# Optimization experiments

Measured on AMD Instinct MI355X. Metric: run time of the kernel, lower is better.

Reference implementation:

```python
import jax, jax.numpy as jnp
import numpy as np

DIM = 256
HEADS = 8
HEAD_DIM = DIM // HEADS
WS = 7            # window size
SHIFT = 3         # shift size
H = 56
W = 56
B = 32
WA = WS * WS      # window area = 49
NWH, NWW = H // WS, W // WS
NW = NWH * NWW    # windows per image


def _make_attn_mask():
    # replicate the torch mask construction for the shifted windows
    img = np.zeros((H, W), dtype=np.float32)
    cnt = 0
    for hs in (slice(0, -WS), slice(-WS, -SHIFT), slice(-SHIFT, None)):
        for ws_ in (slice(0, -WS), slice(-WS, -SHIFT), slice(-SHIFT, None)):
            img[hs, ws_] = cnt
            cnt += 1
    mw = img.reshape(NWH, WS, NWW, WS).transpose(0, 2, 1, 3).reshape(-1, WA)  # (nW, 49)
    diff = mw[:, None, :] - mw[:, :, None]                                    # (nW, 49, 49)
    return np.where(diff != 0, -100.0, 0.0).astype(np.float32)


def _make_rel_index():
    coords = np.stack(np.meshgrid(np.arange(WS), np.arange(WS), indexing='ij')).reshape(2, -1)
    rel = coords[:, :, None] - coords[:, None, :]        # (2, 49, 49)
    rel = rel.transpose(1, 2, 0) + (WS - 1)              # shift to >= 0
    rel[..., 0] *= 2 * WS - 1
    return rel.sum(-1).astype(np.int32)                  # (49, 49) in [0, 169)


def setup_inputs() -> dict:
    key = jax.random.key(0)
    ks = jax.random.split(key, 12)
    s = 0.02
    inp = {
        'x': jax.random.normal(ks[0], (B, H, W, DIM), dtype=jnp.float32),
        'ln1_w': jnp.ones((DIM,), jnp.float32), 'ln1_b': jnp.zeros((DIM,), jnp.float32),
        'qkv_w': s * jax.random.normal(ks[1], (3 * DIM, DIM), jnp.float32),
        'qkv_b': jnp.zeros((3 * DIM,), jnp.float32),
        'rpb_table': s * jax.random.normal(ks[2], ((2 * WS - 1) ** 2, HEADS), jnp.float32),
        'proj_w': s * jax.random.normal(ks[3], (DIM, DIM), jnp.float32),
        'proj_b': jnp.zeros((DIM,), jnp.float32),
        'ln2_w': jnp.ones((DIM,), jnp.float32), 'ln2_b': jnp.zeros((DIM,), jnp.float32),
        'fc1_w': s * jax.random.normal(ks[4], (4 * DIM, DIM), jnp.float32),
        'fc1_b': jnp.zeros((4 * DIM,), jnp.float32),
        'ln3_w': jnp.ones((4 * DIM,), jnp.float32), 'ln3_b': jnp.zeros((4 * DIM,), jnp.float32),
        'fc2_w': s * jax.random.normal(ks[5], (DIM, 4 * DIM), jnp.float32),
        'fc2_b': jnp.zeros((DIM,), jnp.float32),
        'attn_mask': jnp.asarray(_make_attn_mask()),     # (nW, 49, 49)
        'rel_index': jnp.asarray(_make_rel_index()),     # (49, 49) int32
    }
    return inp


def _ln(x, w, b, eps=1e-5):
    m = jnp.mean(x, axis=-1, keepdims=True)
    v = jnp.mean((x - m) ** 2, axis=-1, keepdims=True)
    return (x - m) * jax.lax.rsqrt(v + eps) * w + b


def reference(x, ln1_w, ln1_b, qkv_w, qkv_b, rpb_table, proj_w, proj_b,
              ln2_w, ln2_b, fc1_w, fc1_b, ln3_w, ln3_b, fc2_w, fc2_b,
              attn_mask, rel_index):
    Bn, Hn, Wn, C = x.shape
    # ---- attention branch ----
    y = _ln(x, ln1_w, ln1_b)
    sh = jnp.roll(y, (-SHIFT, -SHIFT), axis=(1, 2))
    # window partition: (B, H, W, C) -> (B*nW, 49, C)
    win = sh.reshape(Bn, NWH, WS, NWW, WS, C).transpose(0, 1, 3, 2, 4, 5).reshape(Bn * NW, WA, C)
    qkv = win @ qkv_w.T + qkv_b                              # (Bw, 49, 3C)
    qkv = qkv.reshape(Bn * NW, WA, 3, HEADS, HEAD_DIM).transpose(2, 0, 3, 1, 4)
    q, k, v = qkv[0], qkv[1], qkv[2]                         # (Bw, h, 49, d)
    scale = HEAD_DIM ** -0.5
    attn = jnp.einsum('bhqd,bhkd->bhqk', q * scale, k)       # (Bw, h, 49, 49)
    bias = rpb_table[rel_index]                              # (49, 49, h)
    attn = attn + jnp.transpose(bias, (2, 0, 1))[None]
    attn = attn.reshape(Bn, NW, HEADS, WA, WA) + attn_mask[None, :, None]
    attn = jax.nn.softmax(attn, axis=-1).reshape(Bn * NW, HEADS, WA, WA)
    out = jnp.einsum('bhqk,bhkd->bhqd', attn, v)             # (Bw, h, 49, d)
    out = out.transpose(0, 2, 1, 3).reshape(Bn * NW, WA, C)
    out = out @ proj_w.T + proj_b
    # window reverse + un-shift
    out = out.reshape(Bn, NWH, NWW, WS, WS, C).transpose(0, 1, 3, 2, 4, 5).reshape(Bn, Hn, Wn, C)
    out = jnp.roll(out, (SHIFT, SHIFT), axis=(1, 2))
    x = x + out
    # ---- MLP branch (note: extra LayerNorm inside MLP per source) ----
    z = _ln(x, ln2_w, ln2_b)
    h = jax.nn.gelu(z @ fc1_w.T + fc1_b, approximate=False)
    h = _ln(h, ln3_w, ln3_b)
    x = x + (h @ fc2_w.T + fc2_b)
    return x
```

## Files before the change

kernel.cpp:

```cpp
#include <hip/hip_runtime.h>
#include <hip/hip_bf16.h>
#include <math.h>

typedef __attribute__((ext_vector_type(8))) short bf16x8;
typedef __attribute__((ext_vector_type(4))) float f32x4;
typedef __attribute__((ext_vector_type(4))) float f4;
typedef __attribute__((ext_vector_type(8))) unsigned short us8;
typedef __attribute__((ext_vector_type(4))) unsigned short us4;
typedef unsigned short u16;
typedef unsigned int u32;

#define HEADS 8
#define SHIFT_ 3
#define HIMG 56
#define WIMG 56
#define WA 49
#define NTOK 100352
#define NPAIR 16384

static __device__ __forceinline__ float bf2f(u16 v){ return __uint_as_float(((u32)v)<<16); }
static __device__ __forceinline__ u16 f2bf(float f){
  u32 u = __float_as_uint(f);
  return (u16)((u + 0x7fffu + ((u>>16)&1u)) >> 16);
}
static __device__ __forceinline__ u32 pkbf(float a, float b){
  __hip_bfloat162 h = __float22bfloat162_rn(make_float2(a, b));
  return *reinterpret_cast<u32*>(&h);
}
static __device__ __forceinline__ float wsum(float v){
  #pragma unroll
  for (int off=32; off>0; off>>=1) v += __shfl_xor(v, off, 64);
  return v;
}
static __device__ __forceinline__ void glds16(const u16* g, u16* l){
  __builtin_amdgcn_global_load_lds(
      (const __attribute__((address_space(1))) unsigned int*)g,
      (__attribute__((address_space(3))) unsigned int*)l, 16, 0, 0);
}
static __device__ __forceinline__ int tok2pix(int row){
  int bw = row / 49, t = row - bw*49;
  int b  = bw >> 6,  w = bw & 63;
  int wh = w >> 3,   ww = w & 7;
  int th = t / 7,    tw = t - th*7;
  int r = wh*7 + th + SHIFT_; if (r >= HIMG) r -= HIMG;
  int c = ww*7 + tw + SHIFT_; if (c >= WIMG) c -= WIMG;
  return (b*HIMG + r)*WIMG + c;
}
static __device__ __forceinline__ float gelu_f(float x){
  float e = __expf(-1.702f*x);
  return x*__builtin_amdgcn_rcpf(1.0f+e);
}

template<int C, int ISBF>
__global__ void ln_stats_kernel(const void* __restrict__ srcv, float* __restrict__ stats){
  int wave = threadIdx.x >> 6, lane = threadIdx.x & 63;
  int tok = blockIdx.x*4 + wave;
  float s=0.f, s2=0.f;
  if (ISBF == 0){
    const float* p = (const float*)srcv + (size_t)tok*C;
    #pragma unroll
    for (int i=0;i<C/256;i++){
      f4 v = *(const f4*)(p + lane*4*(C/256) + i*4);
      #pragma unroll
      for (int e=0;e<4;e++){ float f=v[e]; s+=f; s2+=f*f; }
    }
  } else {
    const u16* p = (const u16*)srcv + (size_t)tok*C;
    #pragma unroll
    for (int i=0;i<C/512;i++){
      us8 v = *(const us8*)(p + lane*8*(C/512) + i*8);
      #pragma unroll
      for (int e=0;e<8;e++){ float f=bf2f(v[e]); s+=f; s2+=f*f; }
    }
  }
  s = wsum(s); s2 = wsum(s2);
  if (lane==0){
    float mean = s/(float)C;
    float var  = s2/(float)C - mean*mean;
    stats[2*tok]   = mean;
    stats[2*tok+1] = rsqrtf(var + 1e-5f);
  }
}

__global__ void ln_apply_kernel(const float* __restrict__ src, u16* __restrict__ dst){
  int wave = threadIdx.x >> 6, lane = threadIdx.x & 63;
  int tok = blockIdx.x*4 + wave;
  const float* p = src + (size_t)tok*256;
  f4 a = *(const f4*)(p + lane*4);
  float s = a[0]+a[1]+a[2]+a[3];
  float s2 = a[0]*a[0]+a[1]*a[1]+a[2]*a[2]+a[3]*a[3];
  s = wsum(s); s2 = wsum(s2);
  float mean = s*(1.f/256.f);
  float var  = s2*(1.f/256.f) - mean*mean;
  float rstd = rsqrtf(var + 1e-5f);
  u32 o2[2];
  o2[0] = pkbf((a[0]-mean)*rstd, (a[1]-mean)*rstd);
  o2[1] = pkbf((a[2]-mean)*rstd, (a[3]-mean)*rstd);
  *(u32*)(dst + (size_t)tok*256 + lane*4)     = o2[0];
  *(u32*)(dst + (size_t)tok*256 + lane*4 + 2) = o2[1];
}

__global__ void ln_apply_b_kernel(const u16* __restrict__ src, u16* __restrict__ dst,
                                  float* __restrict__ st){
  int wave = threadIdx.x >> 6, lane = threadIdx.x & 63;
  int tok = blockIdx.x*4 + wave;
  const u16* p = src + (size_t)tok*256 + lane*4;
  us4 a4 = *(const us4*)p;
  float a0=bf2f(a4[0]), a1=bf2f(a4[1]), a2=bf2f(a4[2]), a3=bf2f(a4[3]);
  float s = a0+a1+a2+a3;
  float s2 = a0*a0+a1*a1+a2*a2+a3*a3;
  s = wsum(s); s2 = wsum(s2);
  float mean = s*(1.f/256.f);
  float var  = s2*(1.f/256.f) - mean*mean;
  float rstd = rsqrtf(var + 1e-5f);
  u32 o0 = pkbf((a0-mean)*rstd, (a1-mean)*rstd);
  u32 o1 = pkbf((a2-mean)*rstd, (a3-mean)*rstd);
  u16* d = dst + (size_t)tok*256 + lane*4;
  *(u32*)d     = o0;
  *(u32*)(d+2) = o1;
  if (lane==0){ st[2*tok] = mean; st[2*tok+1] = rstd; }
}

__global__ void cmb_kernel(const float* __restrict__ rpb, const int* __restrict__ rel,
                           const float* __restrict__ mask, u16* __restrict__ cmb){
  int lin = blockIdx.x*1024 + threadIdx.x*4;
  int j0 = lin & 63;
  int r3 = lin >> 6;
  int i  = r3 % 49;
  int wh = r3 / 49;
  int h = wh & 7, w = wh >> 3;
  us4 o;
  #pragma unroll
  for (int e=0;e<4;e++){
    int j = j0 + e;
    float v = 0.f;
    if (j < WA) v = rpb[rel[i*WA+j]*8 + h] + mask[((size_t)w*WA + i)*WA + j];
    o[e] = f2bf(v);
  }
  *(us4*)(cmb + lin) = o;
}

__global__ void prep_weights(
    const float* __restrict__ qkv_w, const float* __restrict__ qkv_b,
    const float* __restrict__ ln1w,  const float* __restrict__ ln1b,
    const float* __restrict__ fc1_w, const float* __restrict__ fc1_b,
    const float* __restrict__ ln2w,  const float* __restrict__ ln2b,
    const float* __restrict__ fc2_w, const float* __restrict__ fc2_b,
    const float* __restrict__ ln3w,  const float* __restrict__ ln3b,
    const float* __restrict__ proj_w, const float* __restrict__ proj_b,
    u16* __restrict__ wq, float* __restrict__ bq,
    u16* __restrict__ w1, float* __restrict__ b1,
    u16* __restrict__ w2, float* __restrict__ b2,
    u16* __restrict__ wp, float* __restrict__ bp,
    float* __restrict__ cs2, float* __restrict__ hstats)
{
  for (int idx = blockIdx.x*256 + threadIdx.x; idx < 2*NTOK; idx += gridDim.x*256)
    hstats[idx] = 0.f;

  int wave = threadIdx.x>>6, lane = threadIdx.x&63;
  int n = blockIdx.x*4 + wave;
  const float *W,*lw,*lb,*bs; u16* WO; float* BO; int K, row, noln, docs;
  float qs = 1.f;
  if (n < 768)      { W=qkv_w; lw=ln1w; lb=ln1b; bs=qkv_b; WO=wq; BO=bq; K=256;  row=n;      noln=0; docs=0;
                      if (n < 256) qs = 0.17677669529663689f; }
  else if (n < 1792){ W=fc1_w; lw=ln2w; lb=ln2b; bs=fc1_b; WO=w1; BO=b1; K=256;  row=n-768;  noln=0; docs=0; }
  else if (n < 2048){ W=fc2_w; lw=ln3w; lb=ln3b; bs=fc2_b; WO=w2; BO=b2; K=1024; row=n-1792; noln=0; docs=1; }
  else              { W=proj_w; lw=nullptr; lb=nullptr; bs=proj_b; WO=wp; BO=bp; K=256; row=n-2048; noln=1; docs=0; }
  float dot = 0.f, cs = 0.f;
  for (int k=lane; k<K; k+=64){
    float wv = W[(size_t)row*K + k];
    if (noln){
      WO[(size_t)row*K + k] = f2bf(wv);
    } else {
      dot += wv * lb[k];
      u16 q = f2bf(wv * lw[k] * qs);
      WO[(size_t)row*K + k] = q;
      cs += bf2f(q);
    }
  }
  dot = wsum(dot);
  if (docs){ cs = wsum(cs); if (lane==0) cs2[row] = cs; }
  if (lane==0) BO[row] = (bs[row] + dot) * qs;
}

template<int SMODE, int EPI, int SWAP, int DEPTH>
__global__ __launch_bounds__(256)
void gemm18(const void* __restrict__ Av, const u16* __restrict__ Bt,
            const float* __restrict__ stats, float* __restrict__ hstats,
            const float* __restrict__ biasf, const float* __restrict__ resid,
            const float* __restrict__ colsum, void* __restrict__ outv,
            int K, int NT, int CHUNK)
{
  constexpr int BM=128, BN=128, BK=32;
  constexpr int NBUF = DEPTH + 1;
  __shared__ u16 smem[NBUF*8192];
  constexpr int BOFF = NBUF*4096;
  int b = blockIdx.x;
  int linear = (b & 7)*CHUNK + (b >> 3);
  int mt = linear / NT, nt = linear - mt*NT;
  int m0 = mt*BM, n0 = nt*BN;
  int tid  = threadIdx.x;
  int lane = tid & 63, wave = tid >> 6;
  int wr = wave >> 1, wc = wave & 1;
  int lc16 = lane & 15, g = lane >> 4;
  int nsteps = K >> 5;

  const u16* asrc[2];
  const u16* bsrc[2];
  #pragma unroll
  for (int i=0;i<2;i++){
    int c = tid + i*256;
    int row = c >> 2, gch = ((c & 3) - (row >> 1)) & 3;
    if (SMODE <= 1){
      int grow = (SMODE==0) ? tok2pix(m0+row) : (m0+row);
      asrc[i] = (const u16*)Av + (size_t)grow*K + gch*8;
    }
    bsrc[i] = Bt + (size_t)(n0+row)*K + gch*8;
  }
  float smean[2], srstd[2];
  if (SMODE == 3){
    #pragma unroll
    for (int i=0;i<2;i++){
      int grow = m0 + ((tid + i*256) >> 2);
      smean[i] = stats[2*grow]; srstd[i] = stats[2*grow+1];
    }
  }

  f32x4 acc[4][4];
  #pragma unroll
  for (int i=0;i<4;i++)
    #pragma unroll
    for (int j=0;j<4;j++){ acc[i][j][0]=0.f; acc[i][j][1]=0.f; acc[i][j][2]=0.f; acc[i][j][3]=0.f; }

  if (SMODE <= 1){
    #pragma unroll
    for (int pt=0; pt<DEPTH; ++pt){
      int kt = pt << 5;
      #pragma unroll
      for (int i=0;i<2;i++) glds16(asrc[i]+kt, smem + pt*4096 + i*2048 + wave*512);
      #pragma unroll
      for (int i=0;i<2;i++) glds16(bsrc[i]+kt, smem + BOFF + pt*4096 + i*2048 + wave*512);
    }
    if (DEPTH == 3)      asm volatile("s_waitcnt vmcnt(8)" ::: "memory");
    else                 asm volatile("s_waitcnt vmcnt(4)" ::: "memory");
    __builtin_amdgcn_s_barrier();

    int cur = 0;
    for (int t=0; t<nsteps; ++t){
      if (t+DEPTH < nsteps){
        int ktD = (t+DEPTH) << 5;
        int nb = cur + DEPTH; if (nb >= NBUF) nb -= NBUF;
        int off = nb*4096;
        #pragma unroll
        for (int i=0;i<2;i++) glds16(asrc[i]+ktD, smem + off + i*2048 + wave*512);
        #pragma unroll
        for (int i=0;i<2;i++) glds16(bsrc[i]+ktD, smem + BOFF + off + i*2048 + wave*512);
      }
      const u16* Ap = smem + cur*4096;
      const u16* Bp = smem + BOFF + cur*4096;
      bf16x8 af[4], bfr[4];
      #pragma unroll
      for (int mi=0;mi<4;mi++){
        int r = wr*64 + mi*16 + lc16;
        u32 byte = (u32)(r*64) + ((u32)((g + (r>>1)) & 3) << 4);
        af[mi] = *(const bf16x8*)(Ap + (byte>>1));
      }
      #pragma unroll
      for (int ni=0;ni<4;ni++){
        int r = wc*64 + ni*16 + lc16;
        u32 byte = (u32)(r*64) + ((u32)((g + (r>>1)) & 3) << 4);
        bfr[ni] = *(const bf16x8*)(Bp + (byte>>1));
      }
      #pragma unroll
      for (int mi=0;mi<4;mi++)
        #pragma unroll
        for (int ni=0;ni<4;ni++)
          acc[mi][ni] = SWAP ? __builtin_amdgcn_mfma_f32_16x16x32_bf16(bfr[ni], af[mi], acc[mi][ni], 0, 0, 0)
                             : __builtin_amdgcn_mfma_f32_16x16x32_bf16(af[mi], bfr[ni], acc[mi][ni], 0, 0, 0);
      int rem = nsteps - 1 - t;
      int cnt = (rem < DEPTH) ? rem : DEPTH;
      if (cnt >= 3)      asm volatile("s_waitcnt vmcnt(8)" ::: "memory");
      else if (cnt == 2) asm volatile("s_waitcnt vmcnt(4)" ::: "memory");
      else if (cnt == 1) asm volatile("s_waitcnt vmcnt(0)" ::: "memory");
      __builtin_amdgcn_s_barrier();
      cur = (cur+1 == NBUF) ? 0 : cur+1;
    }
  } else {
    f4 rcurf[2][2];
    #pragma unroll
    for (int i=0;i<2;i++){
      int c = tid + i*256; int row = c>>2, gch = ((c&3) - (row>>1)) & 3;
      const float* ap = (const float*)Av + (size_t)(m0+row)*K + gch*8;
      rcurf[i][0] = *(const f4*)ap; rcurf[i][1] = *(const f4*)(ap+4);
    }
    for (int t=0; t<nsteps; ++t){
      int kt = t << 5;
      #pragma unroll
      for (int i=0;i<2;i++){
        int c = tid + i*256; int row = c>>2, s = c&3;
        us8 o;
        #pragma unroll
        for (int e=0;e<8;e++){
          float fv = rcurf[i][e>>2][e&3];
          o[e] = f2bf((fv - smean[i])*srstd[i]);
        }
        u32 byte = (u32)(row*64) + ((u32)s << 4);
        *(us8*)(smem + (byte>>1)) = o;
      }
      #pragma unroll
      for (int i=0;i<2;i++) glds16(bsrc[i]+kt, smem + BOFF + i*2048 + wave*512);
      __syncthreads();
      if (t+1 < nsteps){
        int kt1 = kt + 32;
        #pragma unroll
        for (int i=0;i<2;i++){
          int c = tid + i*256; int row = c>>2, gch = ((c&3) - (row>>1)) & 3;
          const float* ap = (const float*)Av + (size_t)(m0+row)*K + kt1 + gch*8;
          rcurf[i][0] = *(const f4*)ap; rcurf[i][1] = *(const f4*)(ap+4);
        }
      }
      bf16x8 af[4], bfr[4];
      #pragma unroll
      for (int mi=0;mi<4;mi++){
        int r = wr*64 + mi*16 + lc16;
        u32 byte = (u32)(r*64) + ((u32)((g + (r>>1)) & 3) << 4);
        af[mi] = *(const bf16x8*)(smem + (byte>>1));
      }
      #pragma unroll
      for (int ni=0;ni<4;ni++){
        int r = wc*64 + ni*16 + lc16;
        u32 byte = (u32)(r*64) + ((u32)((g + (r>>1)) & 3) << 4);
        bfr[ni] = *(const bf16x8*)(smem + BOFF + (byte>>1));
      }
      #pragma unroll
      for (int mi=0;mi<4;mi++)
        #pragma unroll
        for (int ni=0;ni<4;ni++)
          acc[mi][ni] = SWAP ? __builtin_amdgcn_mfma_f32_16x16x32_bf16(bfr[ni], af[mi], acc[mi][ni], 0, 0, 0)
                             : __builtin_amdgcn_mfma_f32_16x16x32_bf16(af[mi], bfr[ni], acc[mi][ni], 0, 0, 0);
      __syncthreads();
    }
  }

  int lr = lane >> 4;
  if (EPI==0){
    u16* Cs = smem;
    #pragma unroll
    for (int mi=0;mi<4;mi++){
      #pragma unroll
      for (int ni=0;ni<4;ni++){
        int cl = wc*64 + ni*16 + lc16;
        float bv = biasf[n0 + cl];
        #pragma unroll
        for (int j=0;j<4;j++){
          int rl = wr*64 + mi*16 + lr*4 + j;
          float v = acc[mi][ni][j] + bv;
          u32 byte = (u32)(rl*256 + cl*2) ^ ((u32)(rl&7)<<4);
          Cs[byte>>1] = f2bf(v);
        }
      }
    }
    __syncthreads();
    #pragma unroll
    for (int i=0;i<8;i++){
      int c = tid + i*256;
      int rl = c>>4, c0 = (c&15)*8;
      u32 byte = (u32)(rl*256 + c0*2) ^ ((u32)(rl&7)<<4);
      us8 v = *(const us8*)(Cs + (byte>>1));
      int row = m0 + rl, col = n0 + c0;
      int which = col>>8, hh = (col>>5)&7, d0 = col&31;
      int bwi = row/49, t = row - bwi*49;
      *(us8*)((u16*)outv + ((size_t)which*NPAIR + bwi*8 + hh)*(WA*32) + t*32 + d0) = v;
    }
  } else if (EPI==2){
    u16* Cs = smem;
    #pragma unroll
    for (int mi=0;mi<4;mi++){
      int rl = wr*64 + mi*16 + lc16;
      float ss = 0.f, sq = 0.f;
      #pragma unroll
      for (int ni=0;ni<4;ni++){
        int cl = wc*64 + ni*16 + g*4;
        f4 bv = *(const f4*)(biasf + n0 + cl);
        float v0 = gelu_f(acc[mi][ni][0] + bv[0]);
        float v1 = gelu_f(acc[mi][ni][1] + bv[1]);
        float v2 = gelu_f(acc[mi][ni][2] + bv[2]);
        float v3 = gelu_f(acc[mi][ni][3] + bv[3]);
        ss += (v0+v1)+(v2+v3);
        sq += (v0*v0+v1*v1)+(v2*v2+v3*v3);
        u32 w0 = pkbf(v0, v1), w1 = pkbf(v2, v3);
        u32 byte = (u32)(rl*256 + cl*2) ^ ((u32)(rl&7)<<4);
        *(u32*)(Cs + (byte>>1))     = w0;
        *(u32*)(Cs + (byte>>1) + 2) = w1;
      }
      ss += __shfl_xor(ss, 16, 64); ss += __shfl_xor(ss, 32, 64);
      sq += __shfl_xor(sq, 16, 64); sq += __shfl_xor(sq, 32, 64);
      if (g==0){
        int grow = m0 + rl;
        atomicAdd(&hstats[2*grow],   ss);
        atomicAdd(&hstats[2*grow+1], sq);
      }
    }
    __syncthreads();
    #pragma unroll
    for (int i=0;i<8;i++){
      int c = tid + i*256;
      int rl = c>>4, c0 = (c&15)*8;
      u32 byte = (u32)(rl*256 + c0*2) ^ ((u32)(rl&7)<<4);
      us8 v = *(const us8*)(Cs + (byte>>1));
      int row = m0 + rl, col = n0 + c0;
      *(us8*)((u16*)outv + (size_t)row*1024 + col) = v;
    }
  } else if (EPI==5){
    u16* Cs = smem;
    #pragma unroll
    for (int mi=0;mi<4;mi++){
      int rl = wr*64 + mi*16 + lc16;
      int pix = tok2pix(m0 + rl);
      #pragma unroll
      for (int ni=0;ni<4;ni++){
        int cl = wc*64 + ni*16 + g*4;
        int col = n0 + cl;
        f4 bv = *(const f4*)(biasf + col);
        f4 rr = *(const f4*)(resid + (size_t)pix*256 + col);
        float v0 = acc[mi][ni][0] + bv[0] + rr[0];
        float v1 = acc[mi][ni][1] + bv[1] + rr[1];
        float v2 = acc[mi][ni][2] + bv[2] + rr[2];
        float v3 = acc[mi][ni][3] + bv[3] + rr[3];
        u32 w0 = pkbf(v0, v1), w1 = pkbf(v2, v3);
        u32 byte = (u32)(rl*256 + cl*2) ^ ((u32)(rl&7)<<4);
        *(u32*)(Cs + (byte>>1))     = w0;
        *(u32*)(Cs + (byte>>1) + 2) = w1;
      }
    }
    __syncthreads();
    #pragma unroll
    for (int i=0;i<8;i++){
      int c = tid + i*256;
      int rl = c>>4, c0 = (c&15)*8;
      u32 byte = (u32)(rl*256 + c0*2) ^ ((u32)(rl&7)<<4);
      us8 v = *(const us8*)(Cs + (byte>>1));
      int pix = tok2pix(m0 + rl);
      *(us8*)((u16*)outv + (size_t)pix*256 + n0 + c0) = v;
    }
  } else {
    #pragma unroll
    for (int mi=0;mi<4;mi++){
      int rl = wr*64 + mi*16 + lc16;
      int grow = m0 + rl;
      float rs = 1.f, mr = 0.f, istd2 = 0.f, mean2 = 0.f;
      if (EPI==4 || EPI==6){
        float s = stats[2*grow], q = stats[2*grow+1];
        float mean = s*(1.f/1024.f);
        float var  = q*(1.f/1024.f) - mean*mean;
        rs = rsqrtf(var + 1e-5f);
        mr = mean*rs;
      }
      if (EPI==6){
        mean2 = hstats[2*grow];
        istd2 = __builtin_amdgcn_rcpf(hstats[2*grow+1]);
      }
      size_t rowbase = (EPI==1) ? (size_t)tok2pix(grow)*256 : (size_t)grow*256;
      #pragma unroll
      for (int ni=0;ni<4;ni++){
        int col = n0 + wc*64 + ni*16 + g*4;
        f4 bv = *(const f4*)(biasf + col);
        f4 v;
        if (EPI==4 || EPI==6){
          f4 cw = *(const f4*)(colsum + col);
          #pragma unroll
          for (int j=0;j<4;j++) v[j] = acc[mi][ni][j]*rs - mr*cw[j] + bv[j];
        } else {
          #pragma unroll
          for (int j=0;j<4;j++) v[j] = acc[mi][ni][j] + bv[j];
        }
        if (EPI==6){
          us4 xr = *(const us4*)((const u16*)resid + rowbase + col);
          #pragma unroll
          for (int j=0;j<4;j++) v[j] += bf2f(xr[j])*istd2 + mean2;
        } else {
          f4 rr = *(const f4*)(resid + rowbase + col);
          v += rr;
        }
        *(f4*)((float*)outv + rowbase + col) = v;
      }
    }
  }
}

__global__ __launch_bounds__(128)
void attn_mfma_kernel(
    const u16* __restrict__ qkv,
    const u16* __restrict__ cmb,
    u16* __restrict__ outb)
{
  __shared__ u16 smem2[2][12288];
  int wave = threadIdx.x>>6, lane = threadIdx.x&63;
  int pairbase = blockIdx.x*4 + wave*2;
  int bw = pairbase>>3, h0 = pairbase&7, w = bw&63;
  int lc = lane&15, g = lane>>4;
  u16* S = &smem2[wave][0];
  const u16* qg0 = qkv + (size_t)pairbase*(WA*32);
  const u16* qg1 = qg0 + WA*32;
  const u16* kg0 = qg0 + (size_t)NPAIR*(WA*32);
  const u16* kg1 = kg0 + WA*32;
  const u16* vg0 = qg0 + (size_t)2*NPAIR*(WA*32);
  const u16* vg1 = vg0 + WA*32;

  #pragma unroll
  for (int i=0;i<4;i++){
    int idx = i*64 + lane;
    if (idx < 196){
      glds16(kg0 + idx*8, S + idx*8);
      glds16(kg1 + idx*8, S + 2048 + idx*8);
    }
  }
  us8 vv0[4], vv1[4];
  #pragma unroll
  for (int i=0;i<4;i++){
    int idx = i*64+lane; int r = idx>>2, seg = idx&3;
    if (r < WA){
      vv0[i] = *(const us8*)(vg0 + r*32 + seg*8);
      vv1[i] = *(const us8*)(vg1 + r*32 + seg*8);
    } else {
      #pragma unroll
      for (int e=0;e<8;e++){ vv0[i][e]=0; vv1[i][e]=0; }
    }
  }
  bf16x8 qa0[4], qa1[4];
  #pragma unroll
  for (int mi=0;mi<4;mi++){
    int r = mi*16 + lc;
    if (r < WA){
      qa0[mi] = *(const bf16x8*)(qg0 + r*32 + g*8);
      qa1[mi] = *(const bf16x8*)(qg1 + r*32 + g*8);
    } else {
      bf16x8 z;
      #pragma unroll
      for (int e=0;e<8;e++) z[e]=0;
      qa0[mi]=z; qa1[mi]=z;
    }
  }
  #pragma unroll
  for (int i=0;i<4;i++){
    int idx = i*64+lane; int r = idx>>2, seg = idx&3;
    #pragma unroll
    for (int e=0;e<8;e++){
      int d = seg*8 + e;
      u32 byte = ((u32)(d*128 + r*2)) ^ ((u32)(d&7)<<4);
      S[4096 + (byte>>1)] = vv0[i][e];
      S[6144 + (byte>>1)] = vv1[i][e];
    }
  }
  asm volatile("s_waitcnt vmcnt(0)" ::: "memory");
  __builtin_amdgcn_sched_barrier(0);

  u16* Pp = S + 8192;
  #pragma unroll
  for (int p=0; p<2; ++p){
    const u16* Kp = S + p*2048;
    const u16* Vp = S + 4096 + p*2048;
    const u16* cmbp = cmb + ((size_t)((w*8 + h0 + p)*49))*64;

    f32x4 acc[4][4];
    #pragma unroll
    for (int i=0;i<4;i++)
      #pragma unroll
      for (int j=0;j<4;j++){ acc[i][j][0]=0.f; acc[i][j][1]=0.f; acc[i][j][2]=0.f; acc[i][j][3]=0.f; }

    __builtin_amdgcn_s_setprio(1);
    #pragma unroll
    for (int ni=0;ni<4;ni++){
      bf16x8 kb = *(const bf16x8*)(Kp + (ni*16+lc)*32 + g*8);
      #pragma unroll
      for (int mi=0;mi<4;mi++)
        acc[mi][ni] = __builtin_amdgcn_mfma_f32_16x16x32_bf16(p==0 ? qa0[mi] : qa1[mi], kb, acc[mi][ni], 0, 0, 0);
    }
    __builtin_amdgcn_s_setprio(0);

    float rinv[4][4];
    #pragma unroll
    for (int mi=0;mi<4;mi++){
      #pragma unroll
      for (int jr=0;jr<4;jr++){
        int i = mi*16 + g*4 + jr;
        float sv[4];
        #pragma unroll
        for (int ni=0;ni<4;ni++){
          int j = ni*16 + lc;
          float s;
          if (i < WA && j < WA){
            s = acc[mi][ni][jr] + bf2f(cmbp[i*64 + j]);
          } else s = -1e9f;
          sv[ni] = s;
        }
        float mx = fmaxf(fmaxf(sv[0],sv[1]), fmaxf(sv[2],sv[3]));
        #pragma unroll
        for (int off=1; off<16; off<<=1) mx = fmaxf(mx, __shfl_xor(mx, off, 64));
        float sum = 0.f;
        #pragma unroll
        for (int ni=0;ni<4;ni++){ sv[ni] = __expf(sv[ni]-mx); sum += sv[ni]; }
        #pragma unroll
        for (int off=1; off<16; off<<=1) sum += __shfl_xor(sum, off, 64);
        rinv[mi][jr] = __builtin_amdgcn_rcpf(sum);
        #pragma unroll
        for (int ni=0;ni<4;ni++){
          int j = ni*16 + lc;
          u32 byte = ((u32)(i*128 + j*2)) ^ ((u32)(i&7)<<4);
          Pp[byte>>1] = f2bf(sv[ni]);
        }
      }
    }

    bf16x8 vb[2][2];
    #pragma unroll
    for (int kk=0;kk<2;kk++)
      #pragma unroll
      for (int ni=0;ni<2;ni++){
        int d = ni*16 + lc;
        u32 byte = ((u32)(d*128 + kk*64 + g*16)) ^ ((u32)(d&7)<<4);
        vb[kk][ni] = *(const bf16x8*)(Vp + (byte>>1));
      }
    f32x4 aco[4][2];
    #pragma unroll
    for (int i=0;i<4;i++)
      #pragma unroll
      for (int j=0;j<2;j++){ aco[i][j][0]=0.f; aco[i][j][1]=0.f; aco[i][j][2]=0.f; aco[i][j][3]=0.f; }
    __builtin_amdgcn_s_setprio(1);
    #pragma unroll
    for (int mi=0;mi<4;mi++){
      int r = mi*16 + lc;
      #pragma unroll
      for (int kk=0;kk<2;kk++){
        u32 byte = ((u32)(r*128 + kk*64 + g*16)) ^ ((u32)(r&7)<<4);
        bf16x8 pa = *(const bf16x8*)(Pp + (byte>>1));
        #pragma unroll
        for (int ni=0;ni<2;ni++)
          aco[mi][ni] = __builtin_amdgcn_mfma_f32_16x16x32_bf16(pa, vb[kk][ni], aco[mi][ni], 0, 0, 0);
      }
    }
    __builtin_amdgcn_s_setprio(0);

    u16* Op = S + p*2048;
    #pragma unroll
    for (int mi=0;mi<4;mi++){
      #pragma unroll
      for (int jr=0;jr<4;jr++){
        int i = mi*16 + g*4 + jr;
        if (i < WA){
          float rv = rinv[mi][jr];
          #pragma unroll
          for (int ni=0;ni<2;ni++)
            Op[i*32 + ni*16 + lc] = f2bf(aco[mi][ni][jr]*rv);
        }
      }
    }
    size_t obase = (size_t)(bw*WA)*256 + (h0+p)*32;
    #pragma unroll
    for (int i=0;i<4;i++){
      int c = i*64 + lane;
      if (c < WA*4){
        int t = c>>2, seg = c&3;
        *(us8*)(outb + obase + (size_t)t*256 + seg*8) = *(const us8*)(Op + t*32 + seg*8);
      }
    }
  }
}

extern "C" void kernel_launch(void* const* d_in, const int* in_sizes, int n_in,
                              void* d_out, int out_size, void* d_ws, size_t ws_size,
                              hipStream_t stream) {
  const float* x      = (const float*)d_in[0];
  const float* ln1w   = (const float*)d_in[1];
  const float* ln1b   = (const float*)d_in[2];
  const float* qkv_w  = (const float*)d_in[3];
  const float* qkv_b  = (const float*)d_in[4];
  const float* rpb    = (const float*)d_in[5];
  const float* proj_w = (const float*)d_in[6];
  const float* proj_b = (const float*)d_in[7];
  const float* ln2w   = (const float*)d_in[8];
  const float* ln2b   = (const float*)d_in[9];
  const float* fc1_w  = (const float*)d_in[10];
  const float* fc1_b  = (const float*)d_in[11];
  const float* ln3w   = (const float*)d_in[12];
  const float* ln3b   = (const float*)d_in[13];
  const float* fc2_w  = (const float*)d_in[14];
  const float* fc2_b  = (const float*)d_in[15];
  const float* amask  = (const float*)d_in[16];
  const int*   rel    = (const int*)d_in[17];
  float* out = (float*)d_out;

  char* ws = (char*)d_ws;
  float* hstats = (float*)(ws);
  float* stats2 = (float*)(ws +  802816);
  float* bq     = (float*)(ws + 1605632);
  float* b1     = (float*)(ws + 1608704);
  float* b2     = (float*)(ws + 1612800);
  float* bp     = (float*)(ws + 1613824);
  float* cs2    = (float*)(ws + 1614848);
  u16*   wq     = (u16*)  (ws + 1615872);
  u16*   w1     = (u16*)  (ws + 2009088);
  u16*   w2     = (u16*)  (ws + 2533376);
  u16*   wp     = (u16*)  (ws + 3057664);
  const size_t P0 = 3188736;
  u16*   qkvbuf = (u16*)(ws + P0);
  u16*   attno  = (u16*)(ws + P0 + 154140672);
  u16*   xb     = (u16*)(ws + P0 + 154140672);
  u16*   ob     = (u16*)(ws + P0);
  u16*   hbuf   = (u16*)(ws + P0);
  u16*   x1b    = (u16*)(ws + P0 + 205520896);
  u16*   cmb    = (u16*)(ws + P0 + 205520896);
  const int bigws = (ws_size >= (size_t)(P0 + 205520896ull + 51380224ull));

  prep_weights<<<576,256,0,stream>>>(qkv_w,qkv_b,ln1w,ln1b, fc1_w,fc1_b,ln2w,ln2b,
                                     fc2_w,fc2_b,ln3w,ln3b, proj_w,proj_b,
                                     wq,bq, w1,b1, w2,b2, wp,bp, cs2, hstats);
  cmb_kernel<<<1568,256,0,stream>>>(rpb, rel, amask, cmb);
  ln_apply_kernel<<<NTOK/4,256,0,stream>>>(x, xb);
  gemm18<0,0,0,2><<<784*6,256,0,stream>>>(xb, wq, nullptr, nullptr, bq, nullptr, nullptr, qkvbuf, 256, 6, 588);
  attn_mfma_kernel<<<NPAIR/4,128,0,stream>>>(qkvbuf, cmb, attno);
  if (bigws){
    gemm18<1,5,1,2><<<784*2,256,0,stream>>>(attno, wp, nullptr, nullptr, bp, x, nullptr, ob, 256, 2, 196);
    ln_apply_b_kernel<<<NTOK/4,256,0,stream>>>(ob, x1b, stats2);
    gemm18<1,2,1,2><<<784*8,256,0,stream>>>(x1b, w1, nullptr, hstats, b1, nullptr, nullptr, hbuf, 256, 8, 784);
    gemm18<1,6,1,2><<<784*2,256,0,stream>>>(hbuf, w2, hstats, stats2, b2, (const float*)x1b, cs2, out, 1024, 2, 196);
  } else {
    gemm18<1,1,1,2><<<784*2,256,0,stream>>>(attno, wp, nullptr, nullptr, bp, x, nullptr, out, 256, 2, 196);
    ln_stats_kernel<256,0><<<NTOK/4,256,0,stream>>>(out, stats2);
    gemm18<3,2,1,2><<<784*8,256,0,stream>>>(out, w1, stats2, hstats, b1, nullptr, nullptr, (u16*)(ws+P0), 256, 8, 784);
    gemm18<1,4,1,2><<<784*2,256,0,stream>>>((u16*)(ws+P0), w2, hstats, nullptr, b2, out, cs2, out, 1024, 2, 196);
  }
}
```

Baseline: 531.2 us.

## Add 256x128 tile GEMM with 512 threads for MLP fc1/fc2

Introduces gemm19, a GEMM with a 256x128 output tile, 8 waves and a 3-buffer, depth-2 global-to-LDS pipeline, and uses it for the fc1 (GELU + stats) and fc2 (LN-folded residual) GEMMs on the big-workspace path. The larger M tile doubles reuse of the B (weight) tile per block and halves the block count, with the aim of cutting LDS and global traffic per output. The existing gemm18 wait counts are simplified to assume DEPTH 2. The cost is more LDS per block and more threads per block, which may lower occupancy, and the shallower prefetch depth may expose more load latency.

```diff
diff --git a/kernel.cpp b/kernel.cpp
--- a/kernel.cpp
+++ b/kernel.cpp
@@ -241,8 +241,7 @@
       #pragma unroll
       for (int i=0;i<2;i++) glds16(bsrc[i]+kt, smem + BOFF + pt*4096 + i*2048 + wave*512);
     }
-    if (DEPTH == 3)      asm volatile("s_waitcnt vmcnt(8)" ::: "memory");
-    else                 asm volatile("s_waitcnt vmcnt(4)" ::: "memory");
+    asm volatile("s_waitcnt vmcnt(4)" ::: "memory");
     __builtin_amdgcn_s_barrier();
 
     int cur = 0;
@@ -279,8 +278,7 @@
                              : __builtin_amdgcn_mfma_f32_16x16x32_bf16(af[mi], bfr[ni], acc[mi][ni], 0, 0, 0);
       int rem = nsteps - 1 - t;
       int cnt = (rem < DEPTH) ? rem : DEPTH;
-      if (cnt >= 3)      asm volatile("s_waitcnt vmcnt(8)" ::: "memory");
-      else if (cnt == 2) asm volatile("s_waitcnt vmcnt(4)" ::: "memory");
+      if (cnt >= 2)      asm volatile("s_waitcnt vmcnt(4)" ::: "memory");
       else if (cnt == 1) asm volatile("s_waitcnt vmcnt(0)" ::: "memory");
       __builtin_amdgcn_s_barrier();
       cur = (cur+1 == NBUF) ? 0 : cur+1;
@@ -371,6 +369,38 @@
       int which = col>>8, hh = (col>>5)&7, d0 = col&31;
       int bwi = row/49, t = row - bwi*49;
       *(us8*)((u16*)outv + ((size_t)which*NPAIR + bwi*8 + hh)*(WA*32) + t*32 + d0) = v;
+    }
+  } else if (EPI==5){
+    u16* Cs = smem;
+    #pragma unroll
+    for (int mi=0;mi<4;mi++){
+      int rl = wr*64 + mi*16 + lc16;
+      int pix = tok2pix(m0 + rl);
+      #pragma unroll
+      for (int ni=0;ni<4;ni++){
+        int cl = wc*64 + ni*16 + g*4;
+        int col = n0 + cl;
+        f4 bv = *(const f4*)(biasf + col);
+        f4 rr = *(const f4*)(resid + (size_t)pix*256 + col);
+        float v0 = acc[mi][ni][0] + bv[0] + rr[0];
+        float v1 = acc[mi][ni][1] + bv[1] + rr[1];
+        float v2 = acc[mi][ni][2] + bv[2] + rr[2];
+        float v3 = acc[mi][ni][3] + bv[3] + rr[3];
+        u32 w0 = pkbf(v0, v1), w1 = pkbf(v2, v3);
+        u32 byte = (u32)(rl*256 + cl*2) ^ ((u32)(rl&7)<<4);
+        *(u32*)(Cs + (byte>>1))     = w0;
+        *(u32*)(Cs + (byte>>1) + 2) = w1;
+      }
+    }
+    __syncthreads();
+    #pragma unroll
+    for (int i=0;i<8;i++){
+      int c = tid + i*256;
+      int rl = c>>4, c0 = (c&15)*8;
+      u32 byte = (u32)(rl*256 + c0*2) ^ ((u32)(rl&7)<<4);
+      us8 v = *(const us8*)(Cs + (byte>>1));
+      int pix = tok2pix(m0 + rl);
+      *(us8*)((u16*)outv + (size_t)pix*256 + n0 + c0) = v;
     }
   } else if (EPI==2){
     u16* Cs = smem;
@@ -410,38 +440,6 @@
       us8 v = *(const us8*)(Cs + (byte>>1));
       int row = m0 + rl, col = n0 + c0;
       *(us8*)((u16*)outv + (size_t)row*1024 + col) = v;
-    }
-  } else if (EPI==5){
-    u16* Cs = smem;
-    #pragma unroll
-    for (int mi=0;mi<4;mi++){
-      int rl = wr*64 + mi*16 + lc16;
-      int pix = tok2pix(m0 + rl);
-      #pragma unroll
-      for (int ni=0;ni<4;ni++){
-        int cl = wc*64 + ni*16 + g*4;
-        int col = n0 + cl;
-        f4 bv = *(const f4*)(biasf + col);
-        f4 rr = *(const f4*)(resid + (size_t)pix*256 + col);
-        float v0 = acc[mi][ni][0] + bv[0] + rr[0];
-        float v1 = acc[mi][ni][1] + bv[1] + rr[1];
-        float v2 = acc[mi][ni][2] + bv[2] + rr[2];
-        float v3 = acc[mi][ni][3] + bv[3] + rr[3];
-        u32 w0 = pkbf(v0, v1), w1 = pkbf(v2, v3);
-        u32 byte = (u32)(rl*256 + cl*2) ^ ((u32)(rl&7)<<4);
-        *(u32*)(Cs + (byte>>1))     = w0;
-        *(u32*)(Cs + (byte>>1) + 2) = w1;
-      }
-    }
-    __syncthreads();
-    #pragma unroll
-    for (int i=0;i<8;i++){
-      int c = tid + i*256;
-      int rl = c>>4, c0 = (c&15)*8;
-      u32 byte = (u32)(rl*256 + c0*2) ^ ((u32)(rl&7)<<4);
-      us8 v = *(const us8*)(Cs + (byte>>1));
-      int pix = tok2pix(m0 + rl);
-      *(us8*)((u16*)outv + (size_t)pix*256 + n0 + c0) = v;
     }
   } else {
     #pragma unroll
@@ -482,6 +480,161 @@
           f4 rr = *(const f4*)(resid + rowbase + col);
           v += rr;
         }
+        *(f4*)((float*)outv + rowbase + col) = v;
+      }
+    }
+  }
+}
+
+template<int EPI>
+__global__ __launch_bounds__(512)
+void gemm19(const u16* __restrict__ Av, const u16* __restrict__ Bt,
+            const float* __restrict__ stats, float* __restrict__ st2,
+            const float* __restrict__ biasf, const u16* __restrict__ residb,
+            const float* __restrict__ colsum, void* __restrict__ outv,
+            int K, int NT, int CHUNK)
+{
+  constexpr int BM=256, BN=128, BK=32;
+  __shared__ u16 smem[36864];
+  int b = blockIdx.x;
+  int linear = (b & 7)*CHUNK + (b >> 3);
+  int mt = linear / NT, nt = linear - mt*NT;
+  int m0 = mt*BM, n0 = nt*BN;
+  int tid  = threadIdx.x;
+  int lane = tid & 63, wave = tid >> 6;
+  int wr = wave >> 1, wc = wave & 1;
+  int lc16 = lane & 15, g = lane >> 4;
+  int nsteps = K >> 5;
+
+  const u16* asrc[2];
+  #pragma unroll
+  for (int i=0;i<2;i++){
+    int c = tid + i*512;
+    int row = c >> 2, gch = ((c & 3) - (row >> 1)) & 3;
+    asrc[i] = Av + (size_t)(m0+row)*K + gch*8;
+  }
+  const u16* bsrc0;
+  {
+    int row = tid >> 2, gch = ((tid & 3) - (row >> 1)) & 3;
+    bsrc0 = Bt + (size_t)(n0+row)*K + gch*8;
+  }
+
+  f32x4 acc[4][4];
+  #pragma unroll
+  for (int i=0;i<4;i++)
+    #pragma unroll
+    for (int j=0;j<4;j++){ acc[i][j][0]=0.f; acc[i][j][1]=0.f; acc[i][j][2]=0.f; acc[i][j][3]=0.f; }
+
+  #pragma unroll
+  for (int pt=0; pt<2; ++pt){
+    int kt = pt << 5;
+    #pragma unroll
+    for (int i=0;i<2;i++) glds16(asrc[i]+kt, smem + pt*8192 + i*4096 + wave*512);
+    glds16(bsrc0+kt, smem + 24576 + pt*4096 + wave*512);
+  }
+  asm volatile("s_waitcnt vmcnt(3)" ::: "memory");
+  __builtin_amdgcn_s_barrier();
+
+  int cur = 0;
+  for (int t=0; t<nsteps; ++t){
+    if (t+2 < nsteps){
+      int kt2 = (t+2) << 5;
+      int nb = cur + 2; if (nb >= 3) nb -= 3;
+      #pragma unroll
+      for (int i=0;i<2;i++) glds16(asrc[i]+kt2, smem + nb*8192 + i*4096 + wave*512);
+      glds16(bsrc0+kt2, smem + 24576 + nb*4096 + wave*512);
+    }
+    const u16* Ap = smem + cur*8192;
+    const u16* Bp = smem + 24576 + cur*4096;
+    bf16x8 af[4], bfr[4];
+    #pragma unroll
+    for (int mi=0;mi<4;mi++){
+      int r = wr*64 + mi*16 + lc16;
+      u32 byte = (u32)(r*64) + ((u32)((g + (r>>1)) & 3) << 4);
+      af[mi] = *(const bf16x8*)(Ap + (byte>>1));
+    }
+    #pragma unroll
+    for (int ni=0;ni<4;ni++){
+      int r = wc*64 + ni*16 + lc16;
+      u32 byte = (u32)(r*64) + ((u32)((g + (r>>1)) & 3) << 4);
+      bfr[ni] = *(const bf16x8*)(Bp + (byte>>1));
+    }
+    #pragma unroll
+    for (int mi=0;mi<4;mi++)
+      #pragma unroll
+      for (int ni=0;ni<4;ni++)
+        acc[mi][ni] = __builtin_amdgcn_mfma_f32_16x16x32_bf16(bfr[ni], af[mi], acc[mi][ni], 0, 0, 0);
+    int rem = nsteps - 1 - t;
+    int cnt = (rem < 2) ? rem : 2;
+    if (cnt == 2)      asm volatile("s_waitcnt vmcnt(3)" ::: "memory");
+    else if (cnt == 1) asm volatile("s_waitcnt vmcnt(0)" ::: "memory");
+    __builtin_amdgcn_s_barrier();
+    cur = (cur+1 == 3) ? 0 : cur+1;
+  }
+
+  if (EPI==2){
+    u16* Cs = smem;
+    #pragma unroll
+    for (int mi=0;mi<4;mi++){
+      int rl = wr*64 + mi*16 + lc16;
+      float ss = 0.f, sq = 0.f;
+      #pragma unroll
+      for (int ni=0;ni<4;ni++){
+        int cl = wc*64 + ni*16 + g*4;
+        f4 bv = *(const f4*)(biasf + n0 + cl);
+        float v0 = gelu_f(acc[mi][ni][0] + bv[0]);
+        float v1 = gelu_f(acc[mi][ni][1] + bv[1]);
+        float v2 = gelu_f(acc[mi][ni][2] + bv[2]);
+        float v3 = gelu_f(acc[mi][ni][3] + bv[3]);
+        ss += (v0+v1)+(v2+v3);
+        sq += (v0*v0+v1*v1)+(v2*v2+v3*v3);
+        u32 w0 = pkbf(v0, v1), w1 = pkbf(v2, v3);
+        u32 byte = (u32)(rl*256 + cl*2) ^ ((u32)(rl&7)<<4);
+        *(u32*)(Cs + (byte>>1))     = w0;
+        *(u32*)(Cs + (byte>>1) + 2) = w1;
+      }
+      ss += __shfl_xor(ss, 16, 64); ss += __shfl_xor(ss, 32, 64);
+      sq += __shfl_xor(sq, 16, 64); sq += __shfl_xor(sq, 32, 64);
+      if (g==0){
+        int grow = m0 + rl;
+        atomicAdd(&st2[2*grow],   ss);
+        atomicAdd(&st2[2*grow+1], sq);
+      }
+    }
+    __syncthreads();
+    #pragma unroll
+    for (int i=0;i<8;i++){
+      int c = tid + i*512;
+      int rl = c>>4, c0 = (c&15)*8;
+      u32 byte = (u32)(rl*256 + c0*2) ^ ((u32)(rl&7)<<4);
+      us8 v = *(const us8*)(Cs + (byte>>1));
+      int row = m0 + rl, col = n0 + c0;
+      *(us8*)((u16*)outv + (size_t)row*1024 + col) = v;
+    }
+  } else {
+    #pragma unroll
+    for (int mi=0;mi<4;mi++){
+      int rl = wr*64 + mi*16 + lc16;
+      int grow = m0 + rl;
+      float s = stats[2*grow], q = stats[2*grow+1];
+      float mean = s*(1.f/1024.f);
+      float var  = q*(1.f/1024.f) - mean*mean;
+      float rs = rsqrtf(var + 1e-5f);
+      float mr = mean*rs;
+      float mean2 = st2[2*grow];
+      float istd2 = __builtin_amdgcn_rcpf(st2[2*grow+1]);
+      size_t rowbase = (size_t)grow*256;
+      #pragma unroll
+      for (int ni=0;ni<4;ni++){
+        int col = n0 + wc*64 + ni*16 + g*4;
+        f4 bv = *(const f4*)(biasf + col);
+        f4 cw = *(const f4*)(colsum + col);
+        f4 v;
+        #pragma unroll
+        for (int j=0;j<4;j++) v[j] = acc[mi][ni][j]*rs - mr*cw[j] + bv[j];
+        us4 xr = *(const us4*)(residb + rowbase + col);
+        #pragma unroll
+        for (int j=0;j<4;j++) v[j] += bf2f(xr[j])*istd2 + mean2;
         *(f4*)((float*)outv + rowbase + col) = v;
       }
     }
@@ -722,8 +875,8 @@
   if (bigws){
     gemm18<1,5,1,2><<<784*2,256,0,stream>>>(attno, wp, nullptr, nullptr, bp, x, nullptr, ob, 256, 2, 196);
     ln_apply_b_kernel<<<NTOK/4,256,0,stream>>>(ob, x1b, stats2);
-    gemm18<1,2,1,2><<<784*8,256,0,stream>>>(x1b, w1, nullptr, hstats, b1, nullptr, nullptr, hbuf, 256, 8, 784);
-    gemm18<1,6,1,2><<<784*2,256,0,stream>>>(hbuf, w2, hstats, stats2, b2, (const float*)x1b, cs2, out, 1024, 2, 196);
+    gemm19<2><<<3136,512,0,stream>>>(x1b, w1, nullptr, hstats, b1, nullptr, nullptr, hbuf, 256, 8, 392);
+    gemm19<6><<<784,512,0,stream>>>(hbuf, w2, hstats, stats2, b2, x1b, cs2, out, 1024, 2, 98);
   } else {
     gemm18<1,1,1,2><<<784*2,256,0,stream>>>(attno, wp, nullptr, nullptr, bp, x, nullptr, out, 256, 2, 196);
     ln_stats_kernel<256,0><<<NTOK/4,256,0,stream>>>(out, stats2);
```

Measured after the change: 534.6 us. About the same (+0.6%).

## Fuse fc1, GELU, LayerNorm and fc2 into a single MLP kernel

Applied to the files above, without the earlier changes.

Adds mlp_fused, which keeps a 128-row tile of the normalized activations in shared memory. It computes the 1024-wide hidden layer in 128-column chunks with GELU, accumulates the LayerNorm statistics in registers, and feeds each chunk straight into the fc2 accumulation. This removes the round trip of the large hidden buffer through global memory and the atomic statistics pass. In exchange the kernel uses 128 KB of LDS and 512 threads per block, which lowers occupancy, and it only double-buffers weights. The GEMM pipeline wait counts are also simplified so they no longer wait for fewer outstanding loads at depth 3.

```diff
diff --git a/kernel.cpp b/kernel.cpp
--- a/kernel.cpp
+++ b/kernel.cpp
@@ -241,8 +241,7 @@
       #pragma unroll
       for (int i=0;i<2;i++) glds16(bsrc[i]+kt, smem + BOFF + pt*4096 + i*2048 + wave*512);
     }
-    if (DEPTH == 3)      asm volatile("s_waitcnt vmcnt(8)" ::: "memory");
-    else                 asm volatile("s_waitcnt vmcnt(4)" ::: "memory");
+    asm volatile("s_waitcnt vmcnt(4)" ::: "memory");
     __builtin_amdgcn_s_barrier();
 
     int cur = 0;
@@ -279,8 +278,7 @@
                              : __builtin_amdgcn_mfma_f32_16x16x32_bf16(af[mi], bfr[ni], acc[mi][ni], 0, 0, 0);
       int rem = nsteps - 1 - t;
       int cnt = (rem < DEPTH) ? rem : DEPTH;
-      if (cnt >= 3)      asm volatile("s_waitcnt vmcnt(8)" ::: "memory");
-      else if (cnt == 2) asm volatile("s_waitcnt vmcnt(4)" ::: "memory");
+      if (cnt >= 2)      asm volatile("s_waitcnt vmcnt(4)" ::: "memory");
       else if (cnt == 1) asm volatile("s_waitcnt vmcnt(0)" ::: "memory");
       __builtin_amdgcn_s_barrier();
       cur = (cur+1 == NBUF) ? 0 : cur+1;
@@ -371,6 +369,38 @@
       int which = col>>8, hh = (col>>5)&7, d0 = col&31;
       int bwi = row/49, t = row - bwi*49;
       *(us8*)((u16*)outv + ((size_t)which*NPAIR + bwi*8 + hh)*(WA*32) + t*32 + d0) = v;
+    }
+  } else if (EPI==5){
+    u16* Cs = smem;
+    #pragma unroll
+    for (int mi=0;mi<4;mi++){
+      int rl = wr*64 + mi*16 + lc16;
+      int pix = tok2pix(m0 + rl);
+      #pragma unroll
+      for (int ni=0;ni<4;ni++){
+        int cl = wc*64 + ni*16 + g*4;
+        int col = n0 + cl;
+        f4 bv = *(const f4*)(biasf + col);
+        f4 rr = *(const f4*)(resid + (size_t)pix*256 + col);
+        float v0 = acc[mi][ni][0] + bv[0] + rr[0];
+        float v1 = acc[mi][ni][1] + bv[1] + rr[1];
+        float v2 = acc[mi][ni][2] + bv[2] + rr[2];
+        float v3 = acc[mi][ni][3] + bv[3] + rr[3];
+        u32 w0 = pkbf(v0, v1), w1 = pkbf(v2, v3);
+        u32 byte = (u32)(rl*256 + cl*2) ^ ((u32)(rl&7)<<4);
+        *(u32*)(Cs + (byte>>1))     = w0;
+        *(u32*)(Cs + (byte>>1) + 2) = w1;
+      }
+    }
+    __syncthreads();
+    #pragma unroll
+    for (int i=0;i<8;i++){
+      int c = tid + i*256;
+      int rl = c>>4, c0 = (c&15)*8;
+      u32 byte = (u32)(rl*256 + c0*2) ^ ((u32)(rl&7)<<4);
+      us8 v = *(const us8*)(Cs + (byte>>1));
+      int pix = tok2pix(m0 + rl);
+      *(us8*)((u16*)outv + (size_t)pix*256 + n0 + c0) = v;
     }
   } else if (EPI==2){
     u16* Cs = smem;
@@ -411,38 +441,6 @@
       int row = m0 + rl, col = n0 + c0;
       *(us8*)((u16*)outv + (size_t)row*1024 + col) = v;
     }
-  } else if (EPI==5){
-    u16* Cs = smem;
-    #pragma unroll
-    for (int mi=0;mi<4;mi++){
-      int rl = wr*64 + mi*16 + lc16;
-      int pix = tok2pix(m0 + rl);
-      #pragma unroll
-      for (int ni=0;ni<4;ni++){
-        int cl = wc*64 + ni*16 + g*4;
-        int col = n0 + cl;
-        f4 bv = *(const f4*)(biasf + col);
-        f4 rr = *(const f4*)(resid + (size_t)pix*256 + col);
-        float v0 = acc[mi][ni][0] + bv[0] + rr[0];
-        float v1 = acc[mi][ni][1] + bv[1] + rr[1];
-        float v2 = acc[mi][ni][2] + bv[2] + rr[2];
-        float v3 = acc[mi][ni][3] + bv[3] + rr[3];
-        u32 w0 = pkbf(v0, v1), w1 = pkbf(v2, v3);
-        u32 byte = (u32)(rl*256 + cl*2) ^ ((u32)(rl&7)<<4);
-        *(u32*)(Cs + (byte>>1))     = w0;
-        *(u32*)(Cs + (byte>>1) + 2) = w1;
-      }
-    }
-    __syncthreads();
-    #pragma unroll
-    for (int i=0;i<8;i++){
-      int c = tid + i*256;
-      int rl = c>>4, c0 = (c&15)*8;
-      u32 byte = (u32)(rl*256 + c0*2) ^ ((u32)(rl&7)<<4);
-      us8 v = *(const us8*)(Cs + (byte>>1));
-      int pix = tok2pix(m0 + rl);
-      *(us8*)((u16*)outv + (size_t)pix*256 + n0 + c0) = v;
-    }
   } else {
     #pragma unroll
     for (int mi=0;mi<4;mi++){
@@ -484,6 +482,209 @@
         }
         *(f4*)((float*)outv + rowbase + col) = v;
       }
+    }
+  }
+}
+
+__global__ __launch_bounds__(512)
+void mlp_fused(const u16* __restrict__ x1b, const u16* __restrict__ w1,
+               const u16* __restrict__ w2, const float* __restrict__ b1,
+               const float* __restrict__ b2, const float* __restrict__ colsum,
+               const float* __restrict__ st2, float* __restrict__ outv)
+{
+  __shared__ u16 smem[65536];
+  u16* Al = smem;
+  u16* Hl = smem + 32768;
+  u16* Db = smem + 49152;
+
+  int b = blockIdx.x;
+  int linear = (b & 7)*98 + (b >> 3);
+  int m0 = linear * 128;
+  int tid = threadIdx.x;
+  int lane = tid & 63, wave = tid >> 6;
+  int wr = wave >> 2, wcol = wave & 3;
+  int lc16 = lane & 15, g = lane >> 4;
+
+  #pragma unroll
+  for (int i=0;i<8;i++){
+    int c = tid + i*512;
+    int row = c >> 5, s = c & 31, gs = (s - row) & 31;
+    glds16(x1b + (size_t)(m0+row)*256 + gs*8, Al + i*4096 + wave*512);
+  }
+  #pragma unroll
+  for (int i=0;i<2;i++){
+    int c = tid + i*512;
+    int hrow = c >> 3, s = c & 7, gs = (s - hrow) & 7;
+    glds16(w1 + (size_t)hrow*256 + gs*8, Db + i*4096 + wave*512);
+  }
+  asm volatile("s_waitcnt vmcnt(0)" ::: "memory");
+  __builtin_amdgcn_s_barrier();
+
+  f32x4 acc2[4][4];
+  #pragma unroll
+  for (int i=0;i<4;i++)
+    #pragma unroll
+    for (int j=0;j<4;j++){ acc2[i][j][0]=0.f; acc2[i][j][1]=0.f; acc2[i][j][2]=0.f; acc2[i][j][3]=0.f; }
+  float ss[4] = {0.f,0.f,0.f,0.f};
+  float sq[4] = {0.f,0.f,0.f,0.f};
+
+  #pragma unroll 1
+  for (int n=0; n<8; ++n){
+    f32x4 acc1[4][2];
+    #pragma unroll
+    for (int i=0;i<4;i++)
+      #pragma unroll
+      for (int j=0;j<2;j++){ acc1[i][j][0]=0.f; acc1[i][j][1]=0.f; acc1[i][j][2]=0.f; acc1[i][j][3]=0.f; }
+
+    #pragma unroll
+    for (int t=0; t<4; ++t){
+      if (t < 3){
+        #pragma unroll
+        for (int i=0;i<2;i++){
+          int c = tid + i*512;
+          int hrow = c >> 3, s = c & 7, gs = (s - hrow) & 7;
+          glds16(w1 + (size_t)(n*128+hrow)*256 + (t+1)*64 + gs*8,
+                 Db + ((t+1)&1)*8192 + i*4096 + wave*512);
+        }
+      } else {
+        #pragma unroll
+        for (int i=0;i<2;i++){
+          int c = tid + i*512;
+          int crow = c >> 2, s = c & 3, gs = (s - crow) & 3;
+          glds16(w2 + (size_t)crow*1024 + n*128 + gs*8,
+                 Db + i*4096 + wave*512);
+        }
+      }
+      const u16* Bp = Db + (t&1)*8192;
+      #pragma unroll
+      for (int kk=0; kk<2; ++kk){
+        bf16x8 af[4], bff[2];
+        #pragma unroll
+        for (int mi=0;mi<4;mi++){
+          int r = wr*64 + mi*16 + lc16;
+          int gsA = t*8 + kk*4 + g;
+          af[mi] = *(const bf16x8*)(Al + r*256 + ((gsA + r)&31)*8);
+        }
+        #pragma unroll
+        for (int ni=0;ni<2;ni++){
+          int hr = wcol*32 + ni*16 + lc16;
+          bff[ni] = *(const bf16x8*)(Bp + hr*64 + (((kk*4+g) + hr)&7)*8);
+        }
+        #pragma unroll
+        for (int mi=0;mi<4;mi++)
+          #pragma unroll
+          for (int ni=0;ni<2;ni++)
+            acc1[mi][ni] = __builtin_amdgcn_mfma_f32_16x16x32_bf16(bff[ni], af[mi], acc1[mi][ni], 0, 0, 0);
+      }
+      if (t < 3){
+        asm volatile("s_waitcnt vmcnt(0)" ::: "memory");
+        __builtin_amdgcn_s_barrier();
+      } else {
+        #pragma unroll
+        for (int mi=0;mi<4;mi++){
+          int r = wr*64 + mi*16 + lc16;
+          #pragma unroll
+          for (int ni=0;ni<2;ni++){
+            int colh = wcol*32 + ni*16 + g*4;
+            f4 bv = *(const f4*)(b1 + n*128 + colh);
+            float v0 = gelu_f(acc1[mi][ni][0] + bv[0]);
+            float v1 = gelu_f(acc1[mi][ni][1] + bv[1]);
+            float v2 = gelu_f(acc1[mi][ni][2] + bv[2]);
+            float v3 = gelu_f(acc1[mi][ni][3] + bv[3]);
+            ss[mi] += (v0+v1)+(v2+v3);
+            sq[mi] += (v0*v0+v1*v1)+(v2*v2+v3*v3);
+            int off = r*128 + (((wcol*4 + ni*2 + (g>>1)) + r)&15)*8 + (g&1)*4;
+            *(u32*)(Hl + off)     = pkbf(v0, v1);
+            *(u32*)(Hl + off + 2) = pkbf(v2, v3);
+          }
+        }
+        __syncthreads();
+      }
+    }
+
+    #pragma unroll
+    for (int u=0; u<4; ++u){
+      if (u < 3){
+        #pragma unroll
+        for (int i=0;i<2;i++){
+          int c = tid + i*512;
+          int crow = c >> 2, s = c & 3, gs = (s - crow) & 3;
+          glds16(w2 + (size_t)crow*1024 + n*128 + (u+1)*32 + gs*8,
+                 Db + ((u+1)&1)*8192 + i*4096 + wave*512);
+        }
+      } else if (n < 7){
+        #pragma unroll
+        for (int i=0;i<2;i++){
+          int c = tid + i*512;
+          int hrow = c >> 3, s = c & 7, gs = (s - hrow) & 7;
+          glds16(w1 + (size_t)((n+1)*128+hrow)*256 + gs*8,
+                 Db + i*4096 + wave*512);
+        }
+      }
+      const u16* Bp = Db + (u&1)*8192;
+      bf16x8 hf[4], bff[4];
+      #pragma unroll
+      for (int mi=0;mi<4;mi++){
+        int r = wr*64 + mi*16 + lc16;
+        hf[mi] = *(const bf16x8*)(Hl + r*128 + ((u*4 + g + r)&15)*8);
+      }
+      #pragma unroll
+      for (int ni=0;ni<4;ni++){
+        int cr = wcol*64 + ni*16 + lc16;
+        bff[ni] = *(const bf16x8*)(Bp + cr*32 + ((g + cr)&3)*8);
+      }
+      #pragma unroll
+      for (int mi=0;mi<4;mi++)
+        #pragma unroll
+        for (int ni=0;ni<4;ni++)
+          acc2[mi][ni] = __builtin_amdgcn_mfma_f32_16x16x32_bf16(bff[ni], hf[mi], acc2[mi][ni], 0, 0, 0);
+      asm volatile("s_waitcnt vmcnt(0)" ::: "memory");
+      __builtin_amdgcn_s_barrier();
+    }
+  }
+
+  #pragma unroll
+  for (int mi=0;mi<4;mi++){
+    ss[mi] += __shfl_xor(ss[mi], 16, 64); ss[mi] += __shfl_xor(ss[mi], 32, 64);
+    sq[mi] += __shfl_xor(sq[mi], 16, 64); sq[mi] += __shfl_xor(sq[mi], 32, 64);
+  }
+  float* sred = (float*)Hl;
+  if (g == 0){
+    #pragma unroll
+    for (int mi=0;mi<4;mi++){
+      int r = wr*64 + mi*16 + lc16;
+      sred[(wcol*128 + r)*2    ] = ss[mi];
+      sred[(wcol*128 + r)*2 + 1] = sq[mi];
+    }
+  }
+  __syncthreads();
+
+  #pragma unroll
+  for (int mi=0;mi<4;mi++){
+    int r = wr*64 + mi*16 + lc16;
+    int grow = m0 + r;
+    float S = 0.f, Q = 0.f;
+    #pragma unroll
+    for (int wv=0; wv<4; ++wv){ S += sred[(wv*128 + r)*2]; Q += sred[(wv*128 + r)*2 + 1]; }
+    float mean3 = S*(1.f/1024.f);
+    float var3  = Q*(1.f/1024.f) - mean3*mean3;
+    float rs = rsqrtf(var3 + 1e-5f);
+    float mr = mean3 * rs;
+    float mean2 = st2[2*grow];
+    float istd2 = __builtin_amdgcn_rcpf(st2[2*grow+1]);
+    #pragma unroll
+    for (int ni=0;ni<4;ni++){
+      int col = wcol*64 + ni*16 + g*4;
+      f4 bv = *(const f4*)(b2 + col);
+      f4 cw = *(const f4*)(colsum + col);
+      f4 v;
+      #pragma unroll
+      for (int j=0;j<4;j++) v[j] = acc2[mi][ni][j]*rs - mr*cw[j] + bv[j];
+      int aoff = r*256 + (((col>>3) + r)&31)*8 + (col&7);
+      us4 xr = *(const us4*)(Al + aoff);
+      #pragma unroll
+      for (int j=0;j<4;j++) v[j] += bf2f(xr[j])*istd2 + mean2;
+      *(f4*)(outv + (size_t)grow*256 + col) = v;
     }
   }
 }
@@ -707,7 +908,6 @@
   u16*   attno  = (u16*)(ws + P0 + 154140672);
   u16*   xb     = (u16*)(ws + P0 + 154140672);
   u16*   ob     = (u16*)(ws + P0);
-  u16*   hbuf   = (u16*)(ws + P0);
   u16*   x1b    = (u16*)(ws + P0 + 205520896);
   u16*   cmb    = (u16*)(ws + P0 + 205520896);
   const int bigws = (ws_size >= (size_t)(P0 + 205520896ull + 51380224ull));
@@ -722,8 +922,7 @@
   if (bigws){
     gemm18<1,5,1,2><<<784*2,256,0,stream>>>(attno, wp, nullptr, nullptr, bp, x, nullptr, ob, 256, 2, 196);
     ln_apply_b_kernel<<<NTOK/4,256,0,stream>>>(ob, x1b, stats2);
-    gemm18<1,2,1,2><<<784*8,256,0,stream>>>(x1b, w1, nullptr, hstats, b1, nullptr, nullptr, hbuf, 256, 8, 784);
-    gemm18<1,6,1,2><<<784*2,256,0,stream>>>(hbuf, w2, hstats, stats2, b2, (const float*)x1b, cs2, out, 1024, 2, 196);
+    mlp_fused<<<784,512,0,stream>>>(x1b, w1, w2, b1, b2, cs2, stats2, out);
   } else {
     gemm18<1,1,1,2><<<784*2,256,0,stream>>>(attno, wp, nullptr, nullptr, bp, x, nullptr, out, 256, 2, 196);
     ln_stats_kernel<256,0><<<NTOK/4,256,0,stream>>>(out, stats2);
```

Result: no change. 525.1 us (-1.2%).
